# Kernel tuning notes

Hardware: AMD Instinct MI355X
Metric: run time of the kernel (lower is better)

Reference implementation:

```python
import jax, jax.numpy as jnp
import numpy as np

E = 1024      # hidden_size
H = 16        # num_heads
D = E // H    # head_dim = 64
WIN = 256     # window_size
STRIDE = 128
G = 1         # global_tokens
B = 2
L = 4097      # seq_len; local_seq_len = 4096 tiles exactly into 31 windows


def setup_inputs() -> dict:
    key = jax.random.key(0)
    ks = jax.random.split(key, 9)
    s = 0.02
    return {
        "hidden_states": jax.random.normal(ks[0], (B, L, E), jnp.float32),
        "Wq": jax.random.normal(ks[1], (E, E), jnp.float32) * s,
        "bq": jnp.zeros((E,), jnp.float32),
        "Wk": jax.random.normal(ks[2], (E, E), jnp.float32) * s,
        "bk": jnp.zeros((E,), jnp.float32),
        "Wv": jax.random.normal(ks[3], (E, E), jnp.float32) * s,
        "bv": jnp.zeros((E,), jnp.float32),
        "Wo": jax.random.normal(ks[4], (E, E), jnp.float32) * s,
        "bo": jnp.zeros((E,), jnp.float32),
    }


def reference(hidden_states, Wq, bq, Wk, bk, Wv, bv, Wo, bo):
    b, seq_len, e = hidden_states.shape
    scale = 1.0 / jnp.sqrt(jnp.asarray(D, hidden_states.dtype))

    q = (hidden_states @ Wq + bq).reshape(b, seq_len, H, D)
    k = (hidden_states @ Wk + bk).reshape(b, seq_len, H, D)
    v = (hidden_states @ Wv + bv).reshape(b, seq_len, H, D)

    # ---- global tokens attend to the full sequence ----
    qg = q[:, :G]                                        # [b, G, H, D]
    gw = jnp.einsum('bghd,bshd->bhgs', qg, k) * scale    # [b, H, G, L]
    gp = jax.nn.softmax(gw, axis=-1)
    gctx = jnp.einsum('bhgs,bshd->bghd', gp, v).reshape(b, G, e)

    # ---- local windowed attention (overlapping strided windows) ----
    ql, kl, vl = q[:, G:], k[:, G:], v[:, G:]
    Lc = seq_len - G                                     # 4096
    num_windows = max(1, (Lc - WIN) // STRIDE + 1)       # 31
    starts = jnp.arange(num_windows) * STRIDE
    widx = starts[:, None] + jnp.arange(WIN)             # [W, w] window indices

    qw = ql[:, widx]                                     # [b, W, w, H, D]
    kw = kl[:, widx]
    vw = vl[:, widx]
    aw = jnp.einsum('bwqhd,bwkhd->bwhqk', qw, kw) * scale  # [b, W, H, w, w]
    ap = jax.nn.softmax(aw, axis=-1)
    ctx = jnp.einsum('bwhqk,bwkhd->bwqhd', ap, vw)       # [b, W, w, H, D]
    ctx = ctx.reshape(b, num_windows * WIN, e)

    flat = widx.reshape(-1)                              # [W*w]
    local = jnp.zeros((b, Lc, e), hidden_states.dtype).at[:, flat].add(ctx)
    counts = jnp.zeros((Lc,), hidden_states.dtype).at[flat].add(1.0)
    counts = jnp.maximum(counts, 1.0)
    local = local / counts[None, :, None]                # average over overlaps

    out = jnp.concatenate([gctx, local], axis=1)         # [b, L, E]
    return out @ Wo + bo
```

## Files before the change

kernel.cpp:

```cpp
#include <hip/hip_runtime.h>

typedef unsigned short u16;
typedef unsigned int u32;
typedef __bf16 bf16x8 __attribute__((ext_vector_type(8)));
typedef float f4_t __attribute__((ext_vector_type(4)));

#define E_DIM 1024
#define L_TOT 4097
#define B_SZ 2
#define M_ROWS 8194
#define NWIN 31
#define HHEADS 16
#define GCHUNKS 17

__device__ __forceinline__ float b2f(u16 v) {
  union { u32 u; float f; } x; x.u = ((u32)v) << 16; return x.f;
}
__device__ __forceinline__ u16 f2b(float f) {
  union { float f; u32 u; } x; x.f = f;
  u32 r = (x.u + 0x7FFFu + ((x.u >> 16) & 1u)) >> 16;
  return (u16)r;
}
__device__ __forceinline__ f4_t mfma16(bf16x8 a, bf16x8 b, f4_t c) {
  return __builtin_amdgcn_mfma_f32_16x16x32_bf16(a, b, c, 0, 0, 0);
}
__device__ __forceinline__ u32 cvtpk(float lo, float hi) {
  u32 r;
  asm volatile("v_cvt_pk_bf16_f32 %0, %1, %2" : "=v"(r) : "v"(lo), "v"(hi));
  return r;
}

#define GLOAD16(gp, lp)                                                              \
  __builtin_amdgcn_global_load_lds(                                                  \
      (const __attribute__((address_space(1))) u32*)(gp),                            \
      (__attribute__((address_space(3))) u32*)(lp), 16, 0, 0)

#define WAITVM(N) asm volatile("s_waitcnt vmcnt(" #N ")" ::: "memory")
#define WAITLGKM asm volatile("s_waitcnt lgkmcnt(0)" ::: "memory")

__global__ __launch_bounds__(256) void prep_kernel(const float* __restrict__ hs,
                                                   u16* __restrict__ hsb,
                                                   const float* __restrict__ w0,
                                                   const float* __restrict__ w1,
                                                   const float* __restrict__ w2,
                                                   const float* __restrict__ w3,
                                                   u16* __restrict__ wtb) {
  int bid = blockIdx.x;
  if (bid < M_ROWS) {
    int i = bid * 256 + threadIdx.x;
    float4 v = ((const float4*)hs)[i];
    u16 o[4] = {f2b(v.x), f2b(v.y), f2b(v.z), f2b(v.w)};
    *(uint2*)(hsb + (size_t)i * 4) = *(uint2*)o;
  } else {
    int idx2 = bid - M_ROWS;
    int bz = idx2 >> 10;
    int rem = idx2 & 1023;
    int bx = rem & 31, by = rem >> 5;
    const float* src = bz == 0 ? w0 : bz == 1 ? w1 : bz == 2 ? w2 : w3;
    u16* dst = wtb + (size_t)bz * E_DIM * E_DIM;
    __shared__ float tile[32][33];
    int tx = threadIdx.x & 31, ty = threadIdx.x >> 5;
    int x = bx * 32 + tx;
    int y0 = by * 32;
    for (int j = ty; j < 32; j += 8) tile[j][tx] = src[(size_t)(y0 + j) * E_DIM + x];
    __syncthreads();
    for (int j = ty; j < 32; j += 8)
      dst[(size_t)(bx * 32 + j) * E_DIM + by * 32 + tx] = f2b(tile[tx][j]);
  }
}

template <int MODE>
__device__ __forceinline__ void gemmC_body(const u16* __restrict__ A,
                                           const u16* __restrict__ Wt,
                                           const float* __restrict__ b0,
                                           const float* __restrict__ b1,
                                           const float* __restrict__ b2,
                                           void* __restrict__ outBase,
                                           int M) {
  __shared__ __align__(16) char smraw[34816];
  u16* sA = (u16*)smraw;
  u16* sB = sA + 2 * 4096;
  u16* epi16 = (u16*)smraw;
  float* epi32 = (float*)smraw;

  int orig = blockIdx.x;
  int xcd = orig & 7, l = orig >> 3;
  int mt, nt;
  if (MODE == 0) {
    if (l < 192) { mt = (xcd << 3) + (l & 7); nt = l >> 3; }
    else         { mt = 64; nt = xcd * 3 + (l - 192); }
  } else {
    if (l < 64)  { mt = (xcd << 3) + (l & 7); nt = l >> 3; }
    else         { mt = 64; nt = xcd; }
  }
  int m0 = mt * 128, n0 = nt * 128;

  int t = threadIdx.x, lane = t & 63, w = t >> 6;
  int wr = w >> 1, wc = w & 1;
  int lr = lane & 15, g = lane >> 4;

  int ssrc = (((t & 3) ^ ((t >> 3) & 3)) << 3);
  const u16* pa[2];
  const u16* pb[2];
#pragma unroll
  for (int c = 0; c < 2; c++) {
    int ra = m0 + c * 64 + (t >> 2);
    if (ra >= M) ra = M - 1;
    pa[c] = A + (size_t)ra * 1024 + ssrc;
    pb[c] = Wt + (size_t)(n0 + c * 64 + (t >> 2)) * 1024 + ssrc;
  }
  int wb = w * 512;

#define STAGE(bf, ks)                                              \
  {                                                                \
    GLOAD16(pa[0] + (ks) * 32, sA + (bf) * 4096 + wb);             \
    GLOAD16(pa[1] + (ks) * 32, sA + (bf) * 4096 + 2048 + wb);      \
    GLOAD16(pb[0] + (ks) * 32, sB + (bf) * 4096 + wb);             \
    GLOAD16(pb[1] + (ks) * 32, sB + (bf) * 4096 + 2048 + wb);      \
  }

  int swz = ((g ^ ((lr >> 1) & 3)) << 3);
  int arow0 = wr * 64 + lr;
  int brow0 = wc * 64 + lr;

  f4_t acc[4][4] = {};

  STAGE(0, 0);
  STAGE(1, 1);
  WAITVM(4);
  __builtin_amdgcn_s_barrier();
  __builtin_amdgcn_sched_barrier(0);

#pragma unroll 2
  for (int ks = 0; ks < 32; ++ks) {
    int bf = ks & 1;
    int base = bf * 4096;
    bf16x8 av[4], bv[4];
#pragma unroll
    for (int i = 0; i < 4; i++)
      av[i] = *(const bf16x8*)&sA[base + (arow0 + i * 16) * 32 + swz];
#pragma unroll
    for (int j = 0; j < 4; j++)
      bv[j] = *(const bf16x8*)&sB[base + (brow0 + j * 16) * 32 + swz];
    WAITLGKM;
    __builtin_amdgcn_sched_barrier(0);
    __builtin_amdgcn_s_barrier();
    __builtin_amdgcn_sched_barrier(0);
    if (ks < 30) STAGE(bf, ks + 2);
    __builtin_amdgcn_sched_barrier(0);
    __builtin_amdgcn_s_setprio(1);
#pragma unroll
    for (int i = 0; i < 4; i++)
#pragma unroll
      for (int j = 0; j < 4; j++) acc[i][j] = mfma16(av[i], bv[j], acc[i][j]);
    __builtin_amdgcn_s_setprio(0);
    if (ks < 30) {
      WAITVM(4);
    } else if (ks == 30) {
      WAITVM(0);
    }
    if (ks < 31) {
      __builtin_amdgcn_s_barrier();
      __builtin_amdgcn_sched_barrier(0);
    }
  }
  __syncthreads();

  if (MODE == 0) {
    int tsel = n0 >> 10, ncb = n0 & 1023;
    const float* bp = tsel == 0 ? b0 : (tsel == 1 ? b1 : b2);
#pragma unroll
    for (int j = 0; j < 4; j++) {
      int ncl = wc * 64 + j * 16 + lr;
      float bb = bp[ncb + ncl];
#pragma unroll
      for (int i = 0; i < 4; i++) {
        int mlb = wr * 64 + i * 16 + g * 4;
#pragma unroll
        for (int r = 0; r < 4; r++) epi16[(mlb + r) * 136 + ncl] = f2b(acc[i][j][r] + bb);
      }
    }
    __syncthreads();
    int row = t >> 1, half = t & 1;
    int m = m0 + row;
    if (m < M) {
      u16* op = (u16*)outBase + (size_t)tsel * ((size_t)M_ROWS * E_DIM) + (size_t)m * E_DIM + ncb + half * 64;
      const u16* lp = epi16 + row * 136 + half * 64;
#pragma unroll
      for (int qd = 0; qd < 8; qd++) ((uint4*)op)[qd] = ((const uint4*)lp)[qd];
    }
  } else {
#pragma unroll
    for (int p = 0; p < 2; p++) {
      if (p) __syncthreads();
      if (wc == p) {
#pragma unroll
        for (int j = 0; j < 4; j++) {
          int ncl = j * 16 + lr;
          float bb = b0[n0 + p * 64 + ncl];
#pragma unroll
          for (int i = 0; i < 4; i++) {
            int mlb = wr * 64 + i * 16 + g * 4;
#pragma unroll
            for (int r = 0; r < 4; r++) epi32[(mlb + r) * 68 + ncl] = acc[i][j][r] + bb;
          }
        }
      }
      __syncthreads();
      int row = t >> 1, qr = t & 1;
      int m = m0 + row;
      if (m < M) {
        float* op = (float*)outBase + (size_t)m * E_DIM + n0 + p * 64 + qr * 32;
        const float* lp = epi32 + row * 68 + qr * 32;
#pragma unroll
        for (int qd = 0; qd < 8; qd++) ((float4*)op)[qd] = ((const float4*)lp)[qd];
      }
    }
  }
#undef STAGE
}

__global__ __launch_bounds__(256, 4) void gemmC_qkv(const u16* __restrict__ A,
                                                    const u16* __restrict__ Wt,
                                                    const float* __restrict__ b0,
                                                    const float* __restrict__ b1,
                                                    const float* __restrict__ b2,
                                                    void* __restrict__ outBase,
                                                    int M) {
  gemmC_body<0>(A, Wt, b0, b1, b2, outBase, M);
}
__global__ __launch_bounds__(256, 4) void gemmC_out(const u16* __restrict__ A,
                                                    const u16* __restrict__ Wt,
                                                    const float* __restrict__ b0,
                                                    const float* __restrict__ b1,
                                                    const float* __restrict__ b2,
                                                    void* __restrict__ outBase,
                                                    int M) {
  gemmC_body<1>(A, Wt, b0, b1, b2, outBase, M);
}

__global__ __launch_bounds__(256) void gattn1_kernel(const u16* __restrict__ Qb,
                                                     const u16* __restrict__ Kb,
                                                     const u16* __restrict__ Vb,
                                                     float* __restrict__ part) {
  int c = blockIdx.x;
  int h = blockIdx.y;
  int b = blockIdx.z;
  int t = threadIdx.x;
  __shared__ float qsh[64];
  __shared__ float red[4];
  __shared__ float psh[256];
  __shared__ float cred[4][64];

  size_t base = (size_t)b * L_TOT * E_DIM + h * 64;
  if (t < 64) qsh[t] = b2f(Qb[base + t]);
  __syncthreads();

  int row = c * 256 + t;
  bool valid = row < L_TOT;
  float dot = -1e30f;
  if (valid) {
    const u16* kp = Kb + base + (size_t)row * E_DIM;
    float acc = 0.f;
#pragma unroll
    for (int j = 0; j < 64; j += 8) {
      uint4 kv = *(const uint4*)(kp + j);
      const u16* kk = (const u16*)&kv;
#pragma unroll
      for (int q = 0; q < 8; q++) acc += qsh[j + q] * b2f(kk[q]);
    }
    dot = acc * 0.125f;
  }
  float m = dot;
  for (int mask = 1; mask < 64; mask <<= 1) m = fmaxf(m, __shfl_xor(m, mask));
  if ((t & 63) == 0) red[t >> 6] = m;
  __syncthreads();
  m = fmaxf(fmaxf(red[0], red[1]), fmaxf(red[2], red[3]));
  float p = valid ? __expf(dot - m) : 0.f;
  psh[t] = p;
  float s = p;
  for (int mask = 1; mask < 64; mask <<= 1) s += __shfl_xor(s, mask);
  __syncthreads();
  if ((t & 63) == 0) red[t >> 6] = s;
  __syncthreads();
  s = red[0] + red[1] + red[2] + red[3];

  int d = t & 63, gq = t >> 6;
  float acc = 0.f;
#pragma unroll 4
  for (int i = 0; i < 64; i++) {
    int sl = gq * 64 + i;
    int r2 = c * 256 + sl;
    if (r2 < L_TOT) acc += psh[sl] * b2f(Vb[base + (size_t)r2 * E_DIM + d]);
  }
  cred[gq][d] = acc;
  __syncthreads();
  if (t < 64) {
    float v = cred[0][t] + cred[1][t] + cred[2][t] + cred[3][t];
    float* pp = part + (((size_t)(b * HHEADS + h) * GCHUNKS + c) * 66);
    pp[t] = v;
    if (t == 0) { pp[64] = m; pp[65] = s; }
  }
}

#define VT_IDX(d, k) ((d) * 264 + ((k) ^ ((((d) >> 3) & 7) << 3)))
__global__ __launch_bounds__(256) void wattn_kernel(const u16* __restrict__ Qb,
                                                    const u16* __restrict__ Kb,
                                                    const u16* __restrict__ Vb,
                                                    u16* __restrict__ winctx) {
  int wdw = blockIdx.x;
  int h = blockIdx.y;
  int b = blockIdx.z;

  __shared__ __align__(16) u16 Ks[256 * 64];
  __shared__ __align__(16) u16 Vt[64 * 264];

  int t = threadIdx.x, lane = t & 63, wv = t >> 6;
  int g = lane >> 4, lr = lane & 15;
  size_t rowbase = (size_t)b * L_TOT + 1 + (size_t)wdw * 128;
  int hoff = h * 64;

  {
    int rsub = t >> 3;
    int ssrc = ((t & 7) ^ (rsub & 7)) * 8;
    const u16* kp = Kb + (rowbase + rsub) * E_DIM + hoff + ssrc;
#pragma unroll
    for (int c = 0; c < 8; c++)
      GLOAD16(kp + (size_t)c * 32 * E_DIM, Ks + c * 2048 + wv * 512);
  }
#pragma unroll
  for (int rep = 0; rep < 8; rep++) {
    int u = rep * 256 + t;
    int i = u >> 3;
    int d0 = (u & 7) * 8;
    uint4 v = *(const uint4*)(Vb + (rowbase + i) * E_DIM + hoff + d0);
    const u16* pv = (const u16*)&v;
#pragma unroll
    for (int j = 0; j < 8; j++) Vt[VT_IDX(d0 + j, i)] = pv[j];
  }
  __syncthreads();

  int slo = (2 * (g & 1)) * 16 + lr;
  int shi = slo + 16;

  for (int grp = 0; grp < 4; grp++) {
    int q0 = grp * 64 + wv * 16;
    const u16* qp = Qb + (rowbase + q0 + lr) * E_DIM + hoff;
    bf16x8 qa0 = *(const bf16x8*)(qp + g * 8);
    bf16x8 qa1 = *(const bf16x8*)(qp + 32 + g * 8);

    f4_t s[16];
    __builtin_amdgcn_s_setprio(1);
#pragma unroll
    for (int ki = 0; ki < 16; ki++) {
      int row = ki * 16 + lr;
      bf16x8 ka0 = *(const bf16x8*)&Ks[row * 64 + ((g ^ (lr & 7)) << 3)];
      bf16x8 ka1 = *(const bf16x8*)&Ks[row * 64 + (((4 + g) ^ (lr & 7)) << 3)];
      f4_t z = {};
      z = mfma16(ka0, qa0, z);
      z = mfma16(ka1, qa1, z);
      s[ki] = z;
    }
    __builtin_amdgcn_s_setprio(0);

    float mx = -1e30f;
#pragma unroll
    for (int ki = 0; ki < 16; ki++) {
      mx = fmaxf(mx, fmaxf(fmaxf(s[ki][0], s[ki][1]), fmaxf(s[ki][2], s[ki][3])));
    }
    mx = fmaxf(mx, __shfl_xor(mx, 16));
    mx = fmaxf(mx, __shfl_xor(mx, 32));
    float mx8 = mx * 0.125f;
    float sum = 0.f;
    u32 pk[16][2];
#pragma unroll
    for (int ki = 0; ki < 16; ki++) {
      float p0 = __expf(fmaf(s[ki][0], 0.125f, -mx8));
      float p1 = __expf(fmaf(s[ki][1], 0.125f, -mx8));
      float p2 = __expf(fmaf(s[ki][2], 0.125f, -mx8));
      float p3 = __expf(fmaf(s[ki][3], 0.125f, -mx8));
      sum += (p0 + p1) + (p2 + p3);
      pk[ki][0] = cvtpk(p0, p1);
      pk[ki][1] = cvtpk(p2, p3);
    }
    sum += __shfl_xor(sum, 16);
    sum += __shfl_xor(sum, 32);
    float inv = 1.0f / sum;

    u32 paw[8][4];
    bool hi = g >= 2;
#pragma unroll
    for (int kt = 0; kt < 8; kt++) {
      u32 v00 = __shfl((int)pk[kt * 2][0], slo);
      u32 v01 = __shfl((int)pk[kt * 2][1], slo);
      u32 v10 = __shfl((int)pk[kt * 2 + 1][0], slo);
      u32 v11 = __shfl((int)pk[kt * 2 + 1][1], slo);
      u32 w00 = __shfl((int)pk[kt * 2][0], shi);
      u32 w01 = __shfl((int)pk[kt * 2][1], shi);
      u32 w10 = __shfl((int)pk[kt * 2 + 1][0], shi);
      u32 w11 = __shfl((int)pk[kt * 2 + 1][1], shi);
      paw[kt][0] = hi ? v10 : v00;
      paw[kt][1] = hi ? v11 : v01;
      paw[kt][2] = hi ? w10 : w00;
      paw[kt][3] = hi ? w11 : w01;
    }

    f4_t o[4] = {};
    __builtin_amdgcn_s_setprio(1);
#pragma unroll
    for (int dtile = 0; dtile < 4; dtile++) {
      int d = dtile * 16 + lr;
      int dswz = (((d >> 3) & 7) << 3);
#pragma unroll
      for (int kt = 0; kt < 8; kt++) {
        int kphys = (kt * 32 + g * 8) ^ dswz;
        bf16x8 vb = *(const bf16x8*)&Vt[d * 264 + kphys];
        o[dtile] = mfma16(*(const bf16x8*)&paw[kt][0], vb, o[dtile]);
      }
    }
    __builtin_amdgcn_s_setprio(0);

    float invr[4];
#pragma unroll
    for (int r = 0; r < 4; r++) invr[r] = __shfl(inv, g * 4 + r);
    size_t orow = (size_t)(b * NWIN + wdw) * 256 + q0;
#pragma unroll
    for (int dtile = 0; dtile < 4; dtile++) {
#pragma unroll
      for (int r = 0; r < 4; r++) {
        winctx[(orow + g * 4 + r) * E_DIM + hoff + dtile * 16 + lr] =
            f2b(o[dtile][r] * invr[r]);
      }
    }
  }
}

__global__ __launch_bounds__(256) void combine2_kernel(const u16* __restrict__ winctx,
                                                       const float* __restrict__ part,
                                                       u16* __restrict__ ctxb) {
  if (blockIdx.x == 4096) {
    for (int i = threadIdx.x; i < 2048; i += 256) {
      int bh = i >> 6, d = i & 63;
      int b = bh >> 4, h = bh & 15;
      const float* pp = part + ((size_t)(b * HHEADS + h) * GCHUNKS) * 66;
      float m = -1e30f;
#pragma unroll
      for (int c = 0; c < GCHUNKS; c++) m = fmaxf(m, pp[c * 66 + 64]);
      float stot = 0.f, acc = 0.f;
#pragma unroll
      for (int c = 0; c < GCHUNKS; c++) {
        float w = __expf(pp[c * 66 + 64] - m);
        stot += pp[c * 66 + 65] * w;
        acc += pp[c * 66 + d] * w;
      }
      ctxb[(size_t)b * L_TOT * E_DIM + h * 64 + d] = f2b(acc / stot);
    }
    return;
  }
  int idx = blockIdx.x * 256 + threadIdx.x;
  int e0 = (idx & 127) * 8;
  int p = (idx >> 7) & 4095;
  int b = idx >> 19;
  int whi = p >> 7;
  if (whi > 30) whi = 30;
  int off_hi = p - whi * 128;
  int wlo = whi - 1;
  bool has_lo = (wlo >= 0) && (off_hi < 128);

  uint4 vhi = *(const uint4*)(winctx + (((size_t)(b * NWIN + whi) * 256 + off_hi) * E_DIM) + e0);
  const u16* ph = (const u16*)&vhi;
  float vals[8];
#pragma unroll
  for (int j = 0; j < 8; j++) vals[j] = b2f(ph[j]);
  if (has_lo) {
    uint4 vlo = *(const uint4*)(winctx + (((size_t)(b * NWIN + wlo) * 256 + off_hi + 128) * E_DIM) + e0);
    const u16* pl = (const u16*)&vlo;
#pragma unroll
    for (int j = 0; j < 8; j++) vals[j] = (vals[j] + b2f(pl[j])) * 0.5f;
  }
  u16 out[8];
#pragma unroll
  for (int j = 0; j < 8; j++) out[j] = f2b(vals[j]);
  *(uint4*)(ctxb + ((size_t)b * L_TOT + 1 + p) * E_DIM + e0) = *(uint4*)out;
}

extern "C" void kernel_launch(void* const* d_in, const int* in_sizes, int n_in,
                              void* d_out, int out_size, void* d_ws, size_t ws_size,
                              hipStream_t stream) {
  const float* hs = (const float*)d_in[0];
  const float* Wq = (const float*)d_in[1];
  const float* bq = (const float*)d_in[2];
  const float* Wk = (const float*)d_in[3];
  const float* bk = (const float*)d_in[4];
  const float* Wv = (const float*)d_in[5];
  const float* bv = (const float*)d_in[6];
  const float* Wo = (const float*)d_in[7];
  const float* bo = (const float*)d_in[8];

  const size_t BLE = (size_t)M_ROWS * E_DIM;
  const size_t BLE_B = BLE * 2;
  const size_t EE = (size_t)E_DIM * E_DIM;

  char* ws = (char*)d_ws;
  u16* hsb = (u16*)(ws);
  u16* wtb = (u16*)(ws + BLE_B);
  u16* qkv = (u16*)(ws + BLE_B + 4 * EE * 2);
  u16* Qb = qkv;
  u16* Kb = qkv + BLE;
  u16* Vb = qkv + 2 * BLE;
  u16* ctxb = (u16*)(ws + BLE_B + 4 * EE * 2 + 3 * BLE_B);
  u16* winctx = (u16*)(ws + BLE_B + 4 * EE * 2 + 4 * BLE_B);
  float* gpart = (float*)(ws + BLE_B + 4 * EE * 2 + 4 * BLE_B +
                          (size_t)B_SZ * NWIN * 256 * E_DIM * 2);

  prep_kernel<<<M_ROWS + 4096, 256, 0, stream>>>(hs, hsb, Wq, Wk, Wv, Wo, wtb);
  gemmC_qkv<<<1560, 256, 0, stream>>>(hsb, wtb, bq, bk, bv, qkv, M_ROWS);
  gattn1_kernel<<<dim3(GCHUNKS, HHEADS, B_SZ), 256, 0, stream>>>(Qb, Kb, Vb, gpart);
  wattn_kernel<<<dim3(NWIN, HHEADS, B_SZ), 256, 0, stream>>>(Qb, Kb, Vb, winctx);
  combine2_kernel<<<4097, 256, 0, stream>>>(winctx, gpart, ctxb);
  gemmC_out<<<520, 256, 0, stream>>>(ctxb, wtb + 3 * EE, bo, bo, bo, d_out, M_ROWS);
}
```

Measured before the change: 215.2 us.

## Double-buffer GEMM register fragments and fuse global/window attention into one launch

The GEMM main loop now prefetches the next k-step's LDS fragments into a second register set while the current step's MFMAs run, with a manually unrolled ping-pong schedule. It waits for all outstanding global loads (vmcnt 0) before each barrier, and occupancy is lowered from 4 to 3 waves per SIMD via launch bounds. The global-token attention and windowed attention kernels are merged into a single launch that dispatches on block id, cutting one launch and letting both kinds of work share the GPU. The costs are higher register pressure and lower occupancy, plus a possibly stricter wait on global loads.

```diff
diff --git a/kernel.cpp b/kernel.cpp
--- a/kernel.cpp
+++ b/kernel.cpp
@@ -37,6 +37,7 @@
 
 #define WAITVM(N) asm volatile("s_waitcnt vmcnt(" #N ")" ::: "memory")
 #define WAITLGKM asm volatile("s_waitcnt lgkmcnt(0)" ::: "memory")
+#define SCHEDB __builtin_amdgcn_sched_barrier(0)
 
 __global__ __launch_bounds__(256) void prep_kernel(const float* __restrict__ hs,
                                                    u16* __restrict__ hsb,
@@ -70,7 +71,7 @@
 }
 
 template <int MODE>
-__device__ __forceinline__ void gemmC_body(const u16* __restrict__ A,
+__device__ __forceinline__ void gemmD_body(const u16* __restrict__ A,
                                            const u16* __restrict__ Wt,
                                            const float* __restrict__ b0,
                                            const float* __restrict__ b1,
@@ -124,46 +125,57 @@
   int brow0 = wc * 64 + lr;
 
   f4_t acc[4][4] = {};
+  bf16x8 fXA[4], fXB[4], fYA[4], fYB[4];
+
+#define READF(DA, DB, bf)                                                     \
+  {                                                                           \
+    int base_ = (bf) * 4096;                                                  \
+    _Pragma("unroll") for (int i_ = 0; i_ < 4; i_++) {                        \
+      DA[i_] = *(const bf16x8*)&sA[base_ + (arow0 + i_ * 16) * 32 + swz];     \
+      DB[i_] = *(const bf16x8*)&sB[base_ + (brow0 + i_ * 16) * 32 + swz];     \
+    }                                                                         \
+  }
+
+#define ITER(ks, CA, CB, NA, NB)                                              \
+  {                                                                           \
+    if ((ks) >= 1) {                                                          \
+      WAITVM(0);                                                              \
+      SCHEDB;                                                                 \
+      __builtin_amdgcn_s_barrier();                                           \
+      SCHEDB;                                                                 \
+    }                                                                         \
+    if ((ks) < 31) READF(NA, NB, ((ks) + 1) & 1);                             \
+    if ((ks) < 30) STAGE((ks) & 1, (ks) + 2);                                 \
+    SCHEDB;                                                                   \
+    __builtin_amdgcn_s_setprio(1);                                            \
+    _Pragma("unroll") for (int i_ = 0; i_ < 4; i_++)                          \
+      _Pragma("unroll") for (int j_ = 0; j_ < 4; j_++)                        \
+          acc[i_][j_] = mfma16(CA[i_], CB[j_], acc[i_][j_]);                  \
+    __builtin_amdgcn_s_setprio(0);                                            \
+    if ((ks) < 31) { WAITLGKM; SCHEDB; }                                      \
+  }
 
   STAGE(0, 0);
   STAGE(1, 1);
   WAITVM(4);
+  SCHEDB;
   __builtin_amdgcn_s_barrier();
-  __builtin_amdgcn_sched_barrier(0);
-
-#pragma unroll 2
-  for (int ks = 0; ks < 32; ++ks) {
-    int bf = ks & 1;
-    int base = bf * 4096;
-    bf16x8 av[4], bv[4];
-#pragma unroll
-    for (int i = 0; i < 4; i++)
-      av[i] = *(const bf16x8*)&sA[base + (arow0 + i * 16) * 32 + swz];
-#pragma unroll
-    for (int j = 0; j < 4; j++)
-      bv[j] = *(const bf16x8*)&sB[base + (brow0 + j * 16) * 32 + swz];
-    WAITLGKM;
-    __builtin_amdgcn_sched_barrier(0);
-    __builtin_amdgcn_s_barrier();
-    __builtin_amdgcn_sched_barrier(0);
-    if (ks < 30) STAGE(bf, ks + 2);
-    __builtin_amdgcn_sched_barrier(0);
-    __builtin_amdgcn_s_setprio(1);
-#pragma unroll
-    for (int i = 0; i < 4; i++)
-#pragma unroll
-      for (int j = 0; j < 4; j++) acc[i][j] = mfma16(av[i], bv[j], acc[i][j]);
-    __builtin_amdgcn_s_setprio(0);
-    if (ks < 30) {
-      WAITVM(4);
-    } else if (ks == 30) {
-      WAITVM(0);
-    }
-    if (ks < 31) {
-      __builtin_amdgcn_s_barrier();
-      __builtin_amdgcn_sched_barrier(0);
-    }
-  }
+  SCHEDB;
+  READF(fXA, fXB, 0);
+  WAITLGKM;
+  WAITVM(0);
+  SCHEDB;
+  __builtin_amdgcn_s_barrier();
+  SCHEDB;
+
+  ITER(0, fXA, fXB, fYA, fYB);
+  for (int kk = 1; kk <= 27; kk += 2) {
+    ITER(kk, fYA, fYB, fXA, fXB);
+    ITER(kk + 1, fXA, fXB, fYA, fYB);
+  }
+  ITER(29, fYA, fYB, fXA, fXB);
+  ITER(30, fXA, fXB, fYA, fYB);
+  ITER(31, fYA, fYB, fXA, fXB);
   __syncthreads();
 
   if (MODE == 0) {
@@ -218,104 +230,109 @@
     }
   }
 #undef STAGE
-}
-
-__global__ __launch_bounds__(256, 4) void gemmC_qkv(const u16* __restrict__ A,
+#undef READF
+#undef ITER
+}
+
+__global__ __launch_bounds__(256, 3) void gemmD_qkv(const u16* __restrict__ A,
                                                     const u16* __restrict__ Wt,
                                                     const float* __restrict__ b0,
                                                     const float* __restrict__ b1,
                                                     const float* __restrict__ b2,
                                                     void* __restrict__ outBase,
                                                     int M) {
-  gemmC_body<0>(A, Wt, b0, b1, b2, outBase, M);
-}
-__global__ __launch_bounds__(256, 4) void gemmC_out(const u16* __restrict__ A,
+  gemmD_body<0>(A, Wt, b0, b1, b2, outBase, M);
+}
+__global__ __launch_bounds__(256, 3) void gemmD_out(const u16* __restrict__ A,
                                                     const u16* __restrict__ Wt,
                                                     const float* __restrict__ b0,
                                                     const float* __restrict__ b1,
                                                     const float* __restrict__ b2,
                                                     void* __restrict__ outBase,
                                                     int M) {
-  gemmC_body<1>(A, Wt, b0, b1, b2, outBase, M);
-}
-
-__global__ __launch_bounds__(256) void gattn1_kernel(const u16* __restrict__ Qb,
-                                                     const u16* __restrict__ Kb,
-                                                     const u16* __restrict__ Vb,
-                                                     float* __restrict__ part) {
-  int c = blockIdx.x;
-  int h = blockIdx.y;
-  int b = blockIdx.z;
+  gemmD_body<1>(A, Wt, b0, b1, b2, outBase, M);
+}
+
+#define VT_IDX(d, k) ((d) * 264 + ((k) ^ ((((d) >> 3) & 7) << 3)))
+__global__ __launch_bounds__(256) void attn_fused(const u16* __restrict__ Qb,
+                                                  const u16* __restrict__ Kb,
+                                                  const u16* __restrict__ Vb,
+                                                  float* __restrict__ part,
+                                                  u16* __restrict__ winctx) {
+  __shared__ __align__(16) char smem[66560];
+  int bid = blockIdx.x;
   int t = threadIdx.x;
-  __shared__ float qsh[64];
-  __shared__ float red[4];
-  __shared__ float psh[256];
-  __shared__ float cred[4][64];
-
-  size_t base = (size_t)b * L_TOT * E_DIM + h * 64;
-  if (t < 64) qsh[t] = b2f(Qb[base + t]);
-  __syncthreads();
-
-  int row = c * 256 + t;
-  bool valid = row < L_TOT;
-  float dot = -1e30f;
-  if (valid) {
-    const u16* kp = Kb + base + (size_t)row * E_DIM;
+
+  if (bid < 544) {
+    int c = bid % GCHUNKS;
+    int rem = bid / GCHUNKS;
+    int h = rem & 15, b = rem >> 4;
+    float* qsh = (float*)smem;
+    float* red = qsh + 64;
+    float* psh = red + 4;
+    float* cred = psh + 256;
+
+    size_t base = (size_t)b * L_TOT * E_DIM + h * 64;
+    if (t < 64) qsh[t] = b2f(Qb[base + t]);
+    __syncthreads();
+
+    int row = c * 256 + t;
+    bool valid = row < L_TOT;
+    float dot = -1e30f;
+    if (valid) {
+      const u16* kp = Kb + base + (size_t)row * E_DIM;
+      float acc = 0.f;
+#pragma unroll
+      for (int j = 0; j < 64; j += 8) {
+        uint4 kv = *(const uint4*)(kp + j);
+        const u16* kk = (const u16*)&kv;
+#pragma unroll
+        for (int q = 0; q < 8; q++) acc += qsh[j + q] * b2f(kk[q]);
+      }
+      dot = acc * 0.125f;
+    }
+    float m = dot;
+    for (int mask = 1; mask < 64; mask <<= 1) m = fmaxf(m, __shfl_xor(m, mask));
+    if ((t & 63) == 0) red[t >> 6] = m;
+    __syncthreads();
+    m = fmaxf(fmaxf(red[0], red[1]), fmaxf(red[2], red[3]));
+    float p = valid ? __expf(dot - m) : 0.f;
+    psh[t] = p;
+    float s = p;
+    for (int mask = 1; mask < 64; mask <<= 1) s += __shfl_xor(s, mask);
+    __syncthreads();
+    if ((t & 63) == 0) red[t >> 6] = s;
+    __syncthreads();
+    s = red[0] + red[1] + red[2] + red[3];
+
+    int d = t & 63, gq = t >> 6;
     float acc = 0.f;
-#pragma unroll
-    for (int j = 0; j < 64; j += 8) {
-      uint4 kv = *(const uint4*)(kp + j);
-      const u16* kk = (const u16*)&kv;
-#pragma unroll
-      for (int q = 0; q < 8; q++) acc += qsh[j + q] * b2f(kk[q]);
-    }
-    dot = acc * 0.125f;
-  }
-  float m = dot;
-  for (int mask = 1; mask < 64; mask <<= 1) m = fmaxf(m, __shfl_xor(m, mask));
-  if ((t & 63) == 0) red[t >> 6] = m;
-  __syncthreads();
-  m = fmaxf(fmaxf(red[0], red[1]), fmaxf(red[2], red[3]));
-  float p = valid ? __expf(dot - m) : 0.f;
-  psh[t] = p;
-  float s = p;
-  for (int mask = 1; mask < 64; mask <<= 1) s += __shfl_xor(s, mask);
-  __syncthreads();
-  if ((t & 63) == 0) red[t >> 6] = s;
-  __syncthreads();
-  s = red[0] + red[1] + red[2] + red[3];
-
-  int d = t & 63, gq = t >> 6;
-  float acc = 0.f;
 #pragma unroll 4
-  for (int i = 0; i < 64; i++) {
-    int sl = gq * 64 + i;
-    int r2 = c * 256 + sl;
-    if (r2 < L_TOT) acc += psh[sl] * b2f(Vb[base + (size_t)r2 * E_DIM + d]);
-  }
-  cred[gq][d] = acc;
-  __syncthreads();
-  if (t < 64) {
-    float v = cred[0][t] + cred[1][t] + cred[2][t] + cred[3][t];
-    float* pp = part + (((size_t)(b * HHEADS + h) * GCHUNKS + c) * 66);
-    pp[t] = v;
-    if (t == 0) { pp[64] = m; pp[65] = s; }
-  }
-}
-
-#define VT_IDX(d, k) ((d) * 264 + ((k) ^ ((((d) >> 3) & 7) << 3)))
-__global__ __launch_bounds__(256) void wattn_kernel(const u16* __restrict__ Qb,
-                                                    const u16* __restrict__ Kb,
-                                                    const u16* __restrict__ Vb,
-                                                    u16* __restrict__ winctx) {
-  int wdw = blockIdx.x;
-  int h = blockIdx.y;
-  int b = blockIdx.z;
-
-  __shared__ __align__(16) u16 Ks[256 * 64];
-  __shared__ __align__(16) u16 Vt[64 * 264];
-
-  int t = threadIdx.x, lane = t & 63, wv = t >> 6;
+    for (int i = 0; i < 64; i++) {
+      int sl = gq * 64 + i;
+      int r2 = c * 256 + sl;
+      if (r2 < L_TOT) acc += psh[sl] * b2f(Vb[base + (size_t)r2 * E_DIM + d]);
+    }
+    cred[gq * 64 + d] = acc;
+    __syncthreads();
+    if (t < 64) {
+      float v = cred[t] + cred[64 + t] + cred[128 + t] + cred[192 + t];
+      float* pp = part + (((size_t)(b * HHEADS + h) * GCHUNKS + c) * 66);
+      pp[t] = v;
+      if (t == 0) { pp[64] = m; pp[65] = s; }
+    }
+    return;
+  }
+
+  int id = bid - 544;
+  int wdw = id % NWIN;
+  int rem = id / NWIN;
+  int h = rem & 15, b = rem >> 4;
+
+  u16* Ks = (u16*)smem;
+  u16* Vt = Ks + 256 * 64;
+
+  int lane = t & 63, wv = t >> 6;
   int g = lane >> 4, lr = lane & 15;
   size_t rowbase = (size_t)b * L_TOT + 1 + (size_t)wdw * 128;
   int hoff = h * 64;
@@ -514,9 +531,8 @@
                           (size_t)B_SZ * NWIN * 256 * E_DIM * 2);
 
   prep_kernel<<<M_ROWS + 4096, 256, 0, stream>>>(hs, hsb, Wq, Wk, Wv, Wo, wtb);
-  gemmC_qkv<<<1560, 256, 0, stream>>>(hsb, wtb, bq, bk, bv, qkv, M_ROWS);
-  gattn1_kernel<<<dim3(GCHUNKS, HHEADS, B_SZ), 256, 0, stream>>>(Qb, Kb, Vb, gpart);
-  wattn_kernel<<<dim3(NWIN, HHEADS, B_SZ), 256, 0, stream>>>(Qb, Kb, Vb, winctx);
+  gemmD_qkv<<<1560, 256, 0, stream>>>(hsb, wtb, bq, bk, bv, qkv, M_ROWS);
+  attn_fused<<<1536, 256, 0, stream>>>(Qb, Kb, Vb, gpart, winctx);
   combine2_kernel<<<4097, 256, 0, stream>>>(winctx, gpart, ctxb);
-  gemmC_out<<<520, 256, 0, stream>>>(ctxb, wtb + 3 * EE, bo, bo, bo, d_out, M_ROWS);
-}
+  gemmD_out<<<520, 256, 0, stream>>>(ctxb, wtb + 3 * EE, bo, bo, bo, d_out, M_ROWS);
+}
```

Result: no change. 216.0 us (+0.4%).

## Fuse fp32-to-bf16 activation cast into QKV GEMM loads and merge attention kernels

Applied to the files above, without the earlier changes.

The QKV GEMM now reads fp32 hidden states directly through registers, converts them to bf16 and writes them to LDS, so the separate hidden-state cast pass and its bf16 round trip through memory are gone. The B operand still uses direct global-to-LDS loads. The global-token and windowed attention kernels are merged into one launch that dispatches on block index, which removes a launch and lets both run at once. The cost is register-staged A loads with more VGPR pressure and explicit waits inside the GEMM main loop, plus twice the global A-read bytes.

```diff
diff --git a/kernel.cpp b/kernel.cpp
--- a/kernel.cpp
+++ b/kernel.cpp
@@ -37,40 +37,31 @@
 
 #define WAITVM(N) asm volatile("s_waitcnt vmcnt(" #N ")" ::: "memory")
 #define WAITLGKM asm volatile("s_waitcnt lgkmcnt(0)" ::: "memory")
-
-__global__ __launch_bounds__(256) void prep_kernel(const float* __restrict__ hs,
-                                                   u16* __restrict__ hsb,
-                                                   const float* __restrict__ w0,
+#define SCHEDB __builtin_amdgcn_sched_barrier(0)
+
+__global__ __launch_bounds__(256) void prep_kernel(const float* __restrict__ w0,
                                                    const float* __restrict__ w1,
                                                    const float* __restrict__ w2,
                                                    const float* __restrict__ w3,
                                                    u16* __restrict__ wtb) {
-  int bid = blockIdx.x;
-  if (bid < M_ROWS) {
-    int i = bid * 256 + threadIdx.x;
-    float4 v = ((const float4*)hs)[i];
-    u16 o[4] = {f2b(v.x), f2b(v.y), f2b(v.z), f2b(v.w)};
-    *(uint2*)(hsb + (size_t)i * 4) = *(uint2*)o;
-  } else {
-    int idx2 = bid - M_ROWS;
-    int bz = idx2 >> 10;
-    int rem = idx2 & 1023;
-    int bx = rem & 31, by = rem >> 5;
-    const float* src = bz == 0 ? w0 : bz == 1 ? w1 : bz == 2 ? w2 : w3;
-    u16* dst = wtb + (size_t)bz * E_DIM * E_DIM;
-    __shared__ float tile[32][33];
-    int tx = threadIdx.x & 31, ty = threadIdx.x >> 5;
-    int x = bx * 32 + tx;
-    int y0 = by * 32;
-    for (int j = ty; j < 32; j += 8) tile[j][tx] = src[(size_t)(y0 + j) * E_DIM + x];
-    __syncthreads();
-    for (int j = ty; j < 32; j += 8)
-      dst[(size_t)(bx * 32 + j) * E_DIM + by * 32 + tx] = f2b(tile[tx][j]);
-  }
+  int idx2 = blockIdx.x;
+  int bz = idx2 >> 10;
+  int rem = idx2 & 1023;
+  int bx = rem & 31, by = rem >> 5;
+  const float* src = bz == 0 ? w0 : bz == 1 ? w1 : bz == 2 ? w2 : w3;
+  u16* dst = wtb + (size_t)bz * E_DIM * E_DIM;
+  __shared__ float tile[32][33];
+  int tx = threadIdx.x & 31, ty = threadIdx.x >> 5;
+  int x = bx * 32 + tx;
+  int y0 = by * 32;
+  for (int j = ty; j < 32; j += 8) tile[j][tx] = src[(size_t)(y0 + j) * E_DIM + x];
+  __syncthreads();
+  for (int j = ty; j < 32; j += 8)
+    dst[(size_t)(bx * 32 + j) * E_DIM + by * 32 + tx] = f2b(tile[tx][j]);
 }
 
 template <int MODE>
-__device__ __forceinline__ void gemmC_body(const u16* __restrict__ A,
+__device__ __forceinline__ void gemmE_body(const void* __restrict__ Asrc,
                                            const u16* __restrict__ Wt,
                                            const float* __restrict__ b0,
                                            const float* __restrict__ b1,
@@ -100,23 +91,49 @@
   int lr = lane & 15, g = lane >> 4;
 
   int ssrc = (((t & 3) ^ ((t >> 3) & 3)) << 3);
-  const u16* pa[2];
+  const float* paf[2];
+  const u16* pab[2];
   const u16* pb[2];
 #pragma unroll
   for (int c = 0; c < 2; c++) {
     int ra = m0 + c * 64 + (t >> 2);
     if (ra >= M) ra = M - 1;
-    pa[c] = A + (size_t)ra * 1024 + ssrc;
+    if (MODE == 0) paf[c] = (const float*)Asrc + (size_t)ra * 1024 + ssrc;
+    else           pab[c] = (const u16*)Asrc + (size_t)ra * 1024 + ssrc;
     pb[c] = Wt + (size_t)(n0 + c * 64 + (t >> 2)) * 1024 + ssrc;
   }
   int wb = w * 512;
-
-#define STAGE(bf, ks)                                              \
-  {                                                                \
-    GLOAD16(pa[0] + (ks) * 32, sA + (bf) * 4096 + wb);             \
-    GLOAD16(pa[1] + (ks) * 32, sA + (bf) * 4096 + 2048 + wb);      \
-    GLOAD16(pb[0] + (ks) * 32, sB + (bf) * 4096 + wb);             \
-    GLOAD16(pb[1] + (ks) * 32, sB + (bf) * 4096 + 2048 + wb);      \
+  int lslot = wb + lane * 8;
+
+  float4 rA[2][2];
+
+#define AISSUE(ks)                                                      \
+  {                                                                     \
+    rA[0][0] = *(const float4*)(paf[0] + (ks) * 32);                    \
+    rA[0][1] = *(const float4*)(paf[0] + (ks) * 32 + 4);                \
+    rA[1][0] = *(const float4*)(paf[1] + (ks) * 32);                    \
+    rA[1][1] = *(const float4*)(paf[1] + (ks) * 32 + 4);                \
+  }
+#define AWRITE(bf)                                                      \
+  {                                                                     \
+    _Pragma("unroll") for (int c_ = 0; c_ < 2; c_++) {                  \
+      u16 o_[8];                                                        \
+      o_[0] = f2b(rA[c_][0].x); o_[1] = f2b(rA[c_][0].y);               \
+      o_[2] = f2b(rA[c_][0].z); o_[3] = f2b(rA[c_][0].w);               \
+      o_[4] = f2b(rA[c_][1].x); o_[5] = f2b(rA[c_][1].y);               \
+      o_[6] = f2b(rA[c_][1].z); o_[7] = f2b(rA[c_][1].w);               \
+      *(uint4*)(sA + (bf) * 4096 + c_ * 2048 + lslot) = *(uint4*)o_;    \
+    }                                                                   \
+  }
+#define STAGEB(bf, ks)                                              \
+  {                                                                 \
+    GLOAD16(pb[0] + (ks) * 32, sB + (bf) * 4096 + wb);              \
+    GLOAD16(pb[1] + (ks) * 32, sB + (bf) * 4096 + 2048 + wb);       \
+  }
+#define STAGEA_DMA(bf, ks)                                          \
+  {                                                                 \
+    GLOAD16(pab[0] + (ks) * 32, sA + (bf) * 4096 + wb);             \
+    GLOAD16(pab[1] + (ks) * 32, sA + (bf) * 4096 + 2048 + wb);      \
   }
 
   int swz = ((g ^ ((lr >> 1) & 3)) << 3);
@@ -125,16 +142,32 @@
 
   f4_t acc[4][4] = {};
 
-  STAGE(0, 0);
-  STAGE(1, 1);
-  WAITVM(4);
+  if (MODE == 0) {
+    AISSUE(0);
+    STAGEB(0, 0);
+    STAGEB(1, 1);
+    WAITVM(4);
+    AWRITE(0);
+    AISSUE(1);
+    WAITVM(0);
+    AWRITE(1);
+    WAITLGKM;
+  } else {
+    STAGEA_DMA(0, 0);
+    STAGEB(0, 0);
+    STAGEA_DMA(1, 1);
+    STAGEB(1, 1);
+    WAITVM(4);
+  }
+  SCHEDB;
   __builtin_amdgcn_s_barrier();
-  __builtin_amdgcn_sched_barrier(0);
+  SCHEDB;
 
 #pragma unroll 2
   for (int ks = 0; ks < 32; ++ks) {
     int bf = ks & 1;
     int base = bf * 4096;
+    if (MODE == 0 && ks < 30) AISSUE(ks + 2);
     bf16x8 av[4], bv[4];
 #pragma unroll
     for (int i = 0; i < 4; i++)
@@ -143,11 +176,14 @@
     for (int j = 0; j < 4; j++)
       bv[j] = *(const bf16x8*)&sB[base + (brow0 + j * 16) * 32 + swz];
     WAITLGKM;
-    __builtin_amdgcn_sched_barrier(0);
+    SCHEDB;
     __builtin_amdgcn_s_barrier();
-    __builtin_amdgcn_sched_barrier(0);
-    if (ks < 30) STAGE(bf, ks + 2);
-    __builtin_amdgcn_sched_barrier(0);
+    SCHEDB;
+    if (ks < 30) {
+      STAGEB(bf, ks + 2);
+      if (MODE == 1) STAGEA_DMA(bf, ks + 2);
+    }
+    SCHEDB;
     __builtin_amdgcn_s_setprio(1);
 #pragma unroll
     for (int i = 0; i < 4; i++)
@@ -155,13 +191,19 @@
       for (int j = 0; j < 4; j++) acc[i][j] = mfma16(av[i], bv[j], acc[i][j]);
     __builtin_amdgcn_s_setprio(0);
     if (ks < 30) {
-      WAITVM(4);
+      if (MODE == 0) {
+        WAITVM(2);
+        AWRITE(bf);
+        WAITLGKM;
+      } else {
+        WAITVM(4);
+      }
     } else if (ks == 30) {
       WAITVM(0);
     }
     if (ks < 31) {
       __builtin_amdgcn_s_barrier();
-      __builtin_amdgcn_sched_barrier(0);
+      SCHEDB;
     }
   }
   __syncthreads();
@@ -217,105 +259,111 @@
       }
     }
   }
-#undef STAGE
-}
-
-__global__ __launch_bounds__(256, 4) void gemmC_qkv(const u16* __restrict__ A,
+#undef AISSUE
+#undef AWRITE
+#undef STAGEB
+#undef STAGEA_DMA
+}
+
+__global__ __launch_bounds__(256, 4) void gemmE_qkv(const float* __restrict__ A,
                                                     const u16* __restrict__ Wt,
                                                     const float* __restrict__ b0,
                                                     const float* __restrict__ b1,
                                                     const float* __restrict__ b2,
                                                     void* __restrict__ outBase,
                                                     int M) {
-  gemmC_body<0>(A, Wt, b0, b1, b2, outBase, M);
-}
-__global__ __launch_bounds__(256, 4) void gemmC_out(const u16* __restrict__ A,
+  gemmE_body<0>(A, Wt, b0, b1, b2, outBase, M);
+}
+__global__ __launch_bounds__(256, 4) void gemmE_out(const u16* __restrict__ A,
                                                     const u16* __restrict__ Wt,
                                                     const float* __restrict__ b0,
                                                     const float* __restrict__ b1,
                                                     const float* __restrict__ b2,
                                                     void* __restrict__ outBase,
                                                     int M) {
-  gemmC_body<1>(A, Wt, b0, b1, b2, outBase, M);
-}
-
-__global__ __launch_bounds__(256) void gattn1_kernel(const u16* __restrict__ Qb,
-                                                     const u16* __restrict__ Kb,
-                                                     const u16* __restrict__ Vb,
-                                                     float* __restrict__ part) {
-  int c = blockIdx.x;
-  int h = blockIdx.y;
-  int b = blockIdx.z;
+  gemmE_body<1>(A, Wt, b0, b1, b2, outBase, M);
+}
+
+#define VT_IDX(d, k) ((d) * 264 + ((k) ^ ((((d) >> 3) & 7) << 3)))
+__global__ __launch_bounds__(256) void attn_fused(const u16* __restrict__ Qb,
+                                                  const u16* __restrict__ Kb,
+                                                  const u16* __restrict__ Vb,
+                                                  float* __restrict__ part,
+                                                  u16* __restrict__ winctx) {
+  __shared__ __align__(16) char smem[66560];
+  int bid = blockIdx.x;
   int t = threadIdx.x;
-  __shared__ float qsh[64];
-  __shared__ float red[4];
-  __shared__ float psh[256];
-  __shared__ float cred[4][64];
-
-  size_t base = (size_t)b * L_TOT * E_DIM + h * 64;
-  if (t < 64) qsh[t] = b2f(Qb[base + t]);
-  __syncthreads();
-
-  int row = c * 256 + t;
-  bool valid = row < L_TOT;
-  float dot = -1e30f;
-  if (valid) {
-    const u16* kp = Kb + base + (size_t)row * E_DIM;
+
+  if (bid < 544) {
+    int c = bid % GCHUNKS;
+    int rem = bid / GCHUNKS;
+    int h = rem & 15, b = rem >> 4;
+    float* qsh = (float*)smem;
+    float* red = qsh + 64;
+    float* psh = red + 4;
+    float* cred = psh + 256;
+
+    size_t base = (size_t)b * L_TOT * E_DIM + h * 64;
+    if (t < 64) qsh[t] = b2f(Qb[base + t]);
+    __syncthreads();
+
+    int row = c * 256 + t;
+    bool valid = row < L_TOT;
+    float dot = -1e30f;
+    if (valid) {
+      const u16* kp = Kb + base + (size_t)row * E_DIM;
+      float acc = 0.f;
+#pragma unroll
+      for (int j = 0; j < 64; j += 8) {
+        uint4 kv = *(const uint4*)(kp + j);
+        const u16* kk = (const u16*)&kv;
+#pragma unroll
+        for (int q = 0; q < 8; q++) acc += qsh[j + q] * b2f(kk[q]);
+      }
+      dot = acc * 0.125f;
+    }
+    float m = dot;
+    for (int mask = 1; mask < 64; mask <<= 1) m = fmaxf(m, __shfl_xor(m, mask));
+    if ((t & 63) == 0) red[t >> 6] = m;
+    __syncthreads();
+    m = fmaxf(fmaxf(red[0], red[1]), fmaxf(red[2], red[3]));
+    float p = valid ? __expf(dot - m) : 0.f;
+    psh[t] = p;
+    float s = p;
+    for (int mask = 1; mask < 64; mask <<= 1) s += __shfl_xor(s, mask);
+    __syncthreads();
+    if ((t & 63) == 0) red[t >> 6] = s;
+    __syncthreads();
+    s = red[0] + red[1] + red[2] + red[3];
+
+    int d = t & 63, gq = t >> 6;
     float acc = 0.f;
-#pragma unroll
-    for (int j = 0; j < 64; j += 8) {
-      uint4 kv = *(const uint4*)(kp + j);
-      const u16* kk = (const u16*)&kv;
-#pragma unroll
-      for (int q = 0; q < 8; q++) acc += qsh[j + q] * b2f(kk[q]);
-    }
-    dot = acc * 0.125f;
-  }
-  float m = dot;
-  for (int mask = 1; mask < 64; mask <<= 1) m = fmaxf(m, __shfl_xor(m, mask));
-  if ((t & 63) == 0) red[t >> 6] = m;
-  __syncthreads();
-  m = fmaxf(fmaxf(red[0], red[1]), fmaxf(red[2], red[3]));
-  float p = valid ? __expf(dot - m) : 0.f;
-  psh[t] = p;
-  float s = p;
-  for (int mask = 1; mask < 64; mask <<= 1) s += __shfl_xor(s, mask);
-  __syncthreads();
-  if ((t & 63) == 0) red[t >> 6] = s;
-  __syncthreads();
-  s = red[0] + red[1] + red[2] + red[3];
-
-  int d = t & 63, gq = t >> 6;
-  float acc = 0.f;
 #pragma unroll 4
-  for (int i = 0; i < 64; i++) {
-    int sl = gq * 64 + i;
-    int r2 = c * 256 + sl;
-    if (r2 < L_TOT) acc += psh[sl] * b2f(Vb[base + (size_t)r2 * E_DIM + d]);
-  }
-  cred[gq][d] = acc;
-  __syncthreads();
-  if (t < 64) {
-    float v = cred[0][t] + cred[1][t] + cred[2][t] + cred[3][t];
-    float* pp = part + (((size_t)(b * HHEADS + h) * GCHUNKS + c) * 66);
-    pp[t] = v;
-    if (t == 0) { pp[64] = m; pp[65] = s; }
-  }
-}
-
-#define VT_IDX(d, k) ((d) * 264 + ((k) ^ ((((d) >> 3) & 7) << 3)))
-__global__ __launch_bounds__(256) void wattn_kernel(const u16* __restrict__ Qb,
-                                                    const u16* __restrict__ Kb,
-                                                    const u16* __restrict__ Vb,
-                                                    u16* __restrict__ winctx) {
-  int wdw = blockIdx.x;
-  int h = blockIdx.y;
-  int b = blockIdx.z;
-
-  __shared__ __align__(16) u16 Ks[256 * 64];
-  __shared__ __align__(16) u16 Vt[64 * 264];
-
-  int t = threadIdx.x, lane = t & 63, wv = t >> 6;
+    for (int i = 0; i < 64; i++) {
+      int sl = gq * 64 + i;
+      int r2 = c * 256 + sl;
+      if (r2 < L_TOT) acc += psh[sl] * b2f(Vb[base + (size_t)r2 * E_DIM + d]);
+    }
+    cred[gq * 64 + d] = acc;
+    __syncthreads();
+    if (t < 64) {
+      float v = cred[t] + cred[64 + t] + cred[128 + t] + cred[192 + t];
+      float* pp = part + (((size_t)(b * HHEADS + h) * GCHUNKS + c) * 66);
+      pp[t] = v;
+      if (t == 0) { pp[64] = m; pp[65] = s; }
+    }
+    return;
+  }
+
+  int id = bid - 544;
+  int wdw = id % NWIN;
+  int rem = id / NWIN;
+  int h = rem & 15, b = rem >> 4;
+
+  u16* Ks = (u16*)smem;
+  u16* Vt = Ks + 256 * 64;
+
+  int lane = t & 63, wv = t >> 6;
   int g = lane >> 4, lr = lane & 15;
   size_t rowbase = (size_t)b * L_TOT + 1 + (size_t)wdw * 128;
   int hoff = h * 64;
@@ -502,7 +550,6 @@
   const size_t EE = (size_t)E_DIM * E_DIM;
 
   char* ws = (char*)d_ws;
-  u16* hsb = (u16*)(ws);
   u16* wtb = (u16*)(ws + BLE_B);
   u16* qkv = (u16*)(ws + BLE_B + 4 * EE * 2);
   u16* Qb = qkv;
@@ -513,10 +560,9 @@
   float* gpart = (float*)(ws + BLE_B + 4 * EE * 2 + 4 * BLE_B +
                           (size_t)B_SZ * NWIN * 256 * E_DIM * 2);
 
-  prep_kernel<<<M_ROWS + 4096, 256, 0, stream>>>(hs, hsb, Wq, Wk, Wv, Wo, wtb);
-  gemmC_qkv<<<1560, 256, 0, stream>>>(hsb, wtb, bq, bk, bv, qkv, M_ROWS);
-  gattn1_kernel<<<dim3(GCHUNKS, HHEADS, B_SZ), 256, 0, stream>>>(Qb, Kb, Vb, gpart);
-  wattn_kernel<<<dim3(NWIN, HHEADS, B_SZ), 256, 0, stream>>>(Qb, Kb, Vb, winctx);
+  prep_kernel<<<4096, 256, 0, stream>>>(Wq, Wk, Wv, Wo, wtb);
+  gemmE_qkv<<<1560, 256, 0, stream>>>(hs, wtb, bq, bk, bv, qkv, M_ROWS);
+  attn_fused<<<1536, 256, 0, stream>>>(Qb, Kb, Vb, gpart, winctx);
   combine2_kernel<<<4097, 256, 0, stream>>>(winctx, gpart, ctxb);
-  gemmC_out<<<520, 256, 0, stream>>>(ctxb, wtb + 3 * EE, bo, bo, bo, d_out, M_ROWS);
-}
+  gemmE_out<<<520, 256, 0, stream>>>(ctxb, wtb + 3 * EE, bo, bo, bo, d_out, M_ROWS);
+}
```

New measurement: 289.8 us. +34.7%, slower.
